# Optimization experiments

Measured on AMD Instinct MI355X. Metric: run time of the kernel, lower is better.

Reference implementation:

```python
import jax, jax.numpy as jnp
import numpy as np

IN_CH = 256
INTER_CH = 128
B, H, W = 8, 64, 64


def setup_inputs() -> dict:
    key = jax.random.key(0)
    ks = jax.random.split(key, 9)
    s_in = 1.0 / np.sqrt(IN_CH)
    s_int = 1.0 / np.sqrt(INTER_CH)
    return {
        "x": jax.random.normal(ks[0], (B, IN_CH, H, W), dtype=jnp.float32),
        "g_w": jax.random.normal(ks[1], (INTER_CH, IN_CH), dtype=jnp.float32) * s_in,
        "g_b": jax.random.normal(ks[2], (INTER_CH,), dtype=jnp.float32) * s_in,
        "theta_w": jax.random.normal(ks[3], (INTER_CH, IN_CH), dtype=jnp.float32) * s_in,
        "theta_b": jax.random.normal(ks[4], (INTER_CH,), dtype=jnp.float32) * s_in,
        "phi_w": jax.random.normal(ks[5], (INTER_CH, IN_CH), dtype=jnp.float32) * s_in,
        "phi_b": jax.random.normal(ks[6], (INTER_CH,), dtype=jnp.float32) * s_in,
        "W_w": jax.random.normal(ks[7], (IN_CH, INTER_CH), dtype=jnp.float32) * s_int,
        "W_b": jax.random.normal(ks[8], (IN_CH,), dtype=jnp.float32) * s_int,
    }


def _conv1x1(x, w, b):
    # x: [B,C,H,W], w: [O,C], b: [O] -> [B,O,H,W]
    return jnp.einsum("bchw,oc->bohw", x, w) + b[None, :, None, None]


def reference(x, g_w, g_b, theta_w, theta_b, phi_w, phi_b, W_w, W_b):
    b, c, h, w = x.shape
    n = h * w
    ic = g_w.shape[0]
    # 1x1 conv projections, flattened over spatial positions
    g_x = _conv1x1(x, g_w, g_b).reshape(b, ic, n).transpose(0, 2, 1)      # [B,N,ic]
    theta_x = _conv1x1(x, theta_w, theta_b).reshape(b, ic, n).transpose(0, 2, 1)  # [B,N,ic]
    phi_x = _conv1x1(x, phi_w, phi_b).reshape(b, ic, n)                   # [B,ic,N]
    f = jnp.einsum("bnc,bcm->bnm", theta_x, phi_x)                        # [B,N,N]
    # NOTE: original uses F.softmax(f, dim=1) -> normalize over axis 1 (rows)
    f_div_C = jax.nn.softmax(f, axis=1)
    y = jnp.einsum("bnm,bmc->bnc", f_div_C, g_x)                          # [B,N,ic]
    y = y.transpose(0, 2, 1).reshape(b, ic, h, w)                         # [B,ic,H,W]
    W_y = _conv1x1(y, W_w, W_b)                                           # [B,C,H,W]
    return W_y + x
```

## Files before the change

kernel.cpp:

```cpp
#include <hip/hip_runtime.h>
#include <hip/hip_bf16.h>


#define IC   128
#define CIN  256
#define NPOS 4096
#define NB   8

typedef _Float16 f16;
typedef __attribute__((ext_vector_type(8))) _Float16 f16x8;
typedef __attribute__((ext_vector_type(4))) _Float16 f16x4;
typedef __attribute__((ext_vector_type(4))) float f32x4;
typedef __attribute__((ext_vector_type(4))) float fvec4;
typedef __attribute__((ext_vector_type(2))) unsigned int u32x2;

#define MFMA16(a, b, c) __builtin_amdgcn_mfma_f32_16x16x32_f16((a), (b), (c), 0, 0, 0)
#define EXP2(x) __builtin_amdgcn_exp2f(x)

__global__ __launch_bounds__(256) void k_prep_w(
    const float* __restrict__ gw, const float* __restrict__ tw, const float* __restrict__ pw,
    const float* __restrict__ Ww, f16* __restrict__ wAll, f16* __restrict__ Wc)
{
    const int idx = (blockIdx.x * 256 + threadIdx.x) * 4;
    if (idx < 384 * 256) {
        const int row = idx >> 8, col = idx & 255;
        const float* src = (row < 128) ? (gw + row * 256)
                         : (row < 256) ? (tw + (row - 128) * 256)
                                       : (pw + (row - 256) * 256);
        fvec4 v = *reinterpret_cast<const fvec4*>(src + col);
        f16x4 o = { (f16)v[0], (f16)v[1], (f16)v[2], (f16)v[3] };
        *reinterpret_cast<f16x4*>(wAll + idx) = o;
    } else {
        const int j = idx - 384 * 256;
        fvec4 v = *reinterpret_cast<const fvec4*>(Ww + j);
        f16x4 o = { (f16)v[0], (f16)v[1], (f16)v[2], (f16)v[3] };
        *reinterpret_cast<f16x4*>(Wc + j) = o;
    }
}

__global__ __launch_bounds__(256) void k_split_x(
    const float* __restrict__ x, f16* __restrict__ xT)
{
    __shared__ float tile[64][65];
    const int b  = blockIdx.z;
    const int c0 = blockIdx.y * 64;
    const int n0 = blockIdx.x * 64;
    const int t  = threadIdx.x;
    {
        const int cc = t >> 4, nn = (t & 15) * 4;
        const float* src = x + ((size_t)b * CIN + c0) * NPOS + n0;
#pragma unroll
        for (int p = 0; p < 4; ++p) {
            fvec4 v = *reinterpret_cast<const fvec4*>(src + (size_t)(cc + p * 16) * NPOS + nn);
            tile[cc + p * 16][nn + 0] = v[0];
            tile[cc + p * 16][nn + 1] = v[1];
            tile[cc + p * 16][nn + 2] = v[2];
            tile[cc + p * 16][nn + 3] = v[3];
        }
    }
    __syncthreads();
    {
        const int c4 = (t & 15) * 4, nr = t >> 4;
#pragma unroll
        for (int p = 0; p < 4; ++p) {
            const int n = nr + p * 16;
            f16x4 o = { (f16)tile[c4 + 0][n], (f16)tile[c4 + 1][n],
                        (f16)tile[c4 + 2][n], (f16)tile[c4 + 3][n] };
            *reinterpret_cast<f16x4*>(xT + ((size_t)b * NPOS + n0 + n) * CIN + c0 + c4) = o;
        }
    }
}

__global__ __launch_bounds__(256) void k_proj(
    const f16* __restrict__ xT, const f16* __restrict__ wAll,
    const float* __restrict__ gb, const float* __restrict__ tb, const float* __restrict__ pb,
    f16* __restrict__ th, f16* __restrict__ ph, f16* __restrict__ gT)
{
    const int w    = threadIdx.x >> 6;
    const int lane = threadIdx.x & 63;
    const int lrow = lane & 15;
    const int kg   = lane >> 4;
    const int b    = blockIdx.z;
    const int c0   = blockIdx.y * 64;
    const int n0   = blockIdx.x * 256 + w * 64;

    const f16* X = xT + (size_t)b * NPOS * CIN;

    f32x4 acc[4][4] = {};
#pragma unroll
    for (int ks = 0; ks < 8; ++ks) {
        const int k = ks * 32 + kg * 8;
        f16x8 a[4], bv[4];
#pragma unroll
        for (int i = 0; i < 4; ++i) {
            a[i]  = *reinterpret_cast<const f16x8*>(wAll + (size_t)(c0 + i * 16 + lrow) * CIN + k);
            bv[i] = *reinterpret_cast<const f16x8*>(X + (size_t)(n0 + i * 16 + lrow) * CIN + k);
        }
#pragma unroll
        for (int i = 0; i < 4; ++i)
#pragma unroll
            for (int j = 0; j < 4; ++j)
                acc[i][j] = MFMA16(a[i], bv[j], acc[i][j]);
    }
    const int set = c0 >> 7;
    if (set == 0) {
#pragma unroll
        for (int i = 0; i < 4; ++i) {
            const int c = c0 + i * 16 + kg * 4;
#pragma unroll
            for (int j = 0; j < 4; ++j) {
                const int n = n0 + j * 16 + lrow;
#pragma unroll
                for (int r = 0; r < 4; ++r)
                    gT[((size_t)b * IC + c + r) * NPOS + n] = (f16)(acc[i][j][r] + gb[c + r]);
            }
        }
    } else {
        const float* Bi = (set == 1) ? tb : pb;
        f16* dst = (set == 1) ? th : ph;
        const int cl0 = (c0 & 127);
#pragma unroll
        for (int i = 0; i < 4; ++i) {
            const int c = cl0 + i * 16 + kg * 4;
#pragma unroll
            for (int j = 0; j < 4; ++j) {
                const int n = n0 + j * 16 + lrow;
                f16x4 o = { (f16)(acc[i][j][0] + Bi[c + 0]), (f16)(acc[i][j][1] + Bi[c + 1]),
                            (f16)(acc[i][j][2] + Bi[c + 2]), (f16)(acc[i][j][3] + Bi[c + 3]) };
                *reinterpret_cast<f16x4*>(dst + ((size_t)b * NPOS + n) * IC + c) = o;
            }
        }
    }
}

__global__ __launch_bounds__(256, 4) void k_gemm1(
    const f16* __restrict__ th, const f16* __restrict__ ph,
    f16* __restrict__ Ep, float* __restrict__ lmax, float* __restrict__ lsum, int b0)
{
    __shared__ f16 Alds[128 * 64];
    __shared__ f16 Blds[128 * 64];
    const int t    = threadIdx.x;
    const int w    = t >> 6;
    const int lane = t & 63;
    const int lrow = lane & 15;
    const int kg   = lane >> 4;
    const int wm   = w & 1;
    const int wn   = w >> 1;
    const int swz  = (blockIdx.x & 7) * 512 + (blockIdx.x >> 3);
    const int bi   = swz >> 10;
    const int rest = swz & 1023;
    const int mblk = rest & 31;
    const int nblk = rest >> 5;

    const f16* Ag = ph + (size_t)(b0 + bi) * NPOS * IC + (size_t)(mblk * 128) * IC;
    const f16* Bg = th + (size_t)(b0 + bi) * NPOS * IC + (size_t)(nblk * 128) * IC;

    const int trow = t >> 3;
    const int tc   = t & 7;

    f32x4 acc[4][4] = {};
#pragma unroll
    for (int h = 0; h < 2; ++h) {
        if (h) __syncthreads();
#pragma unroll
        for (int it = 0; it < 4; ++it) {
            const int row = trow + it * 32;
            const int cs  = tc ^ (row & 7);
            *reinterpret_cast<f16x8*>(&Alds[row * 64 + cs * 8]) =
                *reinterpret_cast<const f16x8*>(Ag + (size_t)row * IC + h * 64 + tc * 8);
            *reinterpret_cast<f16x8*>(&Blds[row * 64 + cs * 8]) =
                *reinterpret_cast<const f16x8*>(Bg + (size_t)row * IC + h * 64 + tc * 8);
        }
        __syncthreads();
#pragma unroll
        for (int ks = 0; ks < 2; ++ks) {
            f16x8 a[4], bv[4];
#pragma unroll
            for (int i = 0; i < 4; ++i) {
                const int mr = wm * 64 + i * 16 + lrow;
                const int cs = (ks * 4 + kg) ^ (mr & 7);
                a[i] = *reinterpret_cast<const f16x8*>(&Alds[mr * 64 + cs * 8]);
            }
#pragma unroll
            for (int j = 0; j < 4; ++j) {
                const int nr = wn * 64 + j * 16 + lrow;
                const int cs = (ks * 4 + kg) ^ (nr & 7);
                bv[j] = *reinterpret_cast<const f16x8*>(&Blds[nr * 64 + cs * 8]);
            }
#pragma unroll
            for (int i = 0; i < 4; ++i)
#pragma unroll
                for (int j = 0; j < 4; ++j)
                    acc[i][j] = MFMA16(a[i], bv[j], acc[i][j]);
        }
    }

    const int m0 = mblk * 128 + wm * 64;
    const int n0 = nblk * 128 + wn * 64;
    f16* eb = Ep + (size_t)bi * NPOS * NPOS;
    const float L2E = 1.4426950408889634f;

    f32x4 cm[4], ncml[4];
#pragma unroll
    for (int i = 0; i < 4; ++i)
#pragma unroll
        for (int r = 0; r < 4; ++r) {
            float c = fmaxf(fmaxf(acc[i][0][r], acc[i][1][r]),
                            fmaxf(acc[i][2][r], acc[i][3][r]));
            c = fmaxf(c, __shfl_xor(c, 1));
            c = fmaxf(c, __shfl_xor(c, 2));
            c = fmaxf(c, __shfl_xor(c, 4));
            c = fmaxf(c, __shfl_xor(c, 8));
            cm[i][r] = c;
            ncml[i][r] = -c * L2E;
        }

    f32x4 s[4] = {};
#pragma unroll
    for (int j = 0; j < 4; ++j) {
        f16* rowp = eb + (size_t)(n0 + j * 16 + lrow) * NPOS + m0 + kg * 4;
#pragma unroll
        for (int i = 0; i < 4; ++i) {
            float e0 = EXP2(__builtin_fmaf(acc[i][j][0], L2E, ncml[i][0]));
            float e1 = EXP2(__builtin_fmaf(acc[i][j][1], L2E, ncml[i][1]));
            float e2 = EXP2(__builtin_fmaf(acc[i][j][2], L2E, ncml[i][2]));
            float e3 = EXP2(__builtin_fmaf(acc[i][j][3], L2E, ncml[i][3]));
            s[i][0] += e0; s[i][1] += e1; s[i][2] += e2; s[i][3] += e3;
            u32x2 o = { __builtin_bit_cast(unsigned int, __builtin_amdgcn_cvt_pkrtz(e0, e1)),
                        __builtin_bit_cast(unsigned int, __builtin_amdgcn_cvt_pkrtz(e2, e3)) };
            *reinterpret_cast<u32x2*>(rowp + i * 16) = o;
        }
    }

    const int rowblk = nblk * 2 + wn;
#pragma unroll
    for (int i = 0; i < 4; ++i)
#pragma unroll
        for (int r = 0; r < 4; ++r) {
            float ss = s[i][r];
            ss += __shfl_xor(ss, 1);
            ss += __shfl_xor(ss, 2);
            ss += __shfl_xor(ss, 4);
            ss += __shfl_xor(ss, 8);
            if (lrow == 0) {
                const size_t off = ((size_t)bi * 64 + rowblk) * NPOS + m0 + i * 16 + kg * 4 + r;
                lmax[off] = cm[i][r];
                lsum[off] = ss;
            }
        }
}

__global__ __launch_bounds__(256) void k_prep(
    const float* __restrict__ lmax, const float* __restrict__ lsum,
    const f16* __restrict__ gT, f16* __restrict__ sca, f16* __restrict__ gs, int b0)
{
    const float L2E = 1.4426950408889634f;
    const int bi = blockIdx.y;
    const int m  = blockIdx.x * 256 + threadIdx.x;
    const float* lm = lmax + (size_t)bi * 64 * NPOS;
    const float* ls = lsum + (size_t)bi * 64 * NPOS;
    float cm = -3.0e38f;
#pragma unroll 8
    for (int rb = 0; rb < 64; ++rb)
        cm = fmaxf(cm, lm[(size_t)rb * NPOS + m]);
    float s = 0.f;
    f16* scab = sca + (size_t)bi * 64 * NPOS;
#pragma unroll 8
    for (int rb = 0; rb < 64; ++rb) {
        float e = EXP2((lm[(size_t)rb * NPOS + m] - cm) * L2E);
        s += e * ls[(size_t)rb * NPOS + m];
        scab[(size_t)rb * NPOS + m] = (f16)e;
    }
    const float rc = 1.0f / s;
    const f16* gb = gT + (size_t)(b0 + bi) * IC * NPOS;
    f16* gsb = gs + (size_t)bi * IC * NPOS;
#pragma unroll 8
    for (int c = 0; c < IC; ++c)
        gsb[(size_t)c * NPOS + m] = (f16)((float)gb[(size_t)c * NPOS + m] * rc);
}

__global__ __launch_bounds__(256, 2) void k_gemm2(
    const f16* __restrict__ Ep, const f16* __restrict__ sca,
    const f16* __restrict__ gs, f16* __restrict__ partial)
{
    __shared__ f16 Elds[2][128 * 64];
    __shared__ f16 Glds[2][128 * 64];
    const int t    = threadIdx.x;
    const int w    = t >> 6;
    const int lane = t & 63;
    const int lrow = lane & 15;
    const int kg   = lane >> 4;
    const int wc   = w & 1;
    const int wn   = w >> 1;
    const int swz  = (blockIdx.x & 7) * 64 + (blockIdx.x >> 3);
    const int bi   = swz >> 7;
    const int rest = swz & 127;
    const int kc   = rest & 3;
    const int nblk = rest >> 2;

    const f16* Eg  = Ep + (size_t)bi * NPOS * NPOS + (size_t)(nblk * 128) * NPOS + kc * 1024;
    const f16* Gg  = gs + (size_t)bi * IC * NPOS + kc * 1024;
    const int  rb  = nblk * 2 + wn;
    const f16* srow = sca + ((size_t)bi * 64 + rb) * NPOS + kc * 1024;

    const int trow = t >> 3;
    const int tc   = t & 7;

    f16x8 pe[4], pg[4];
#pragma unroll
    for (int it = 0; it < 4; ++it) {
        const int row = trow + it * 32;
        pe[it] = *reinterpret_cast<const f16x8*>(Eg + (size_t)row * NPOS + tc * 8);
        pg[it] = *reinterpret_cast<const f16x8*>(Gg + (size_t)row * NPOS + tc * 8);
    }

    f32x4 acc[4][4] = {};
    for (int sc = 0; sc < 16; ++sc) {
        const int cur = sc & 1;
#pragma unroll
        for (int it = 0; it < 4; ++it) {
            const int row = trow + it * 32;
            const int cs  = tc ^ (row & 7);
            *reinterpret_cast<f16x8*>(&Elds[cur][row * 64 + cs * 8]) = pe[it];
            *reinterpret_cast<f16x8*>(&Glds[cur][row * 64 + cs * 8]) = pg[it];
        }
        if (sc < 15) {
#pragma unroll
            for (int it = 0; it < 4; ++it) {
                const int row = trow + it * 32;
                pe[it] = *reinterpret_cast<const f16x8*>(Eg + (size_t)row * NPOS + (sc + 1) * 64 + tc * 8);
                pg[it] = *reinterpret_cast<const f16x8*>(Gg + (size_t)row * NPOS + (sc + 1) * 64 + tc * 8);
            }
        }
        __syncthreads();

#pragma unroll
        for (int ks = 0; ks < 2; ++ks) {
            f16x8 sv = *reinterpret_cast<const f16x8*>(srow + sc * 64 + ks * 32 + kg * 8);
            f16x8 a[4], ev[4];
#pragma unroll
            for (int i = 0; i < 4; ++i) {
                const int cr = wc * 64 + i * 16 + lrow;
                const int cs = (ks * 4 + kg) ^ (cr & 7);
                a[i] = *reinterpret_cast<const f16x8*>(&Glds[cur][cr * 64 + cs * 8]);
            }
#pragma unroll
            for (int j = 0; j < 4; ++j) {
                const int nr = wn * 64 + j * 16 + lrow;
                const int cs = (ks * 4 + kg) ^ (nr & 7);
                ev[j] = *reinterpret_cast<const f16x8*>(&Elds[cur][nr * 64 + cs * 8]) * sv;
            }
#pragma unroll
            for (int i = 0; i < 4; ++i)
#pragma unroll
                for (int j = 0; j < 4; ++j)
                    acc[i][j] = MFMA16(a[i], ev[j], acc[i][j]);
        }
    }

    f16* pb = partial + ((size_t)bi * 4 + kc) * NPOS * IC;
    const int n0 = nblk * 128 + wn * 64;
    const int c0 = wc * 64;
#pragma unroll
    for (int j = 0; j < 4; ++j) {
        f16* rowp = pb + (size_t)(n0 + j * 16 + lrow) * IC + c0 + kg * 4;
#pragma unroll
        for (int i = 0; i < 4; ++i) {
            f16x4 o = { (f16)acc[i][j][0], (f16)acc[i][j][1],
                        (f16)acc[i][j][2], (f16)acc[i][j][3] };
            *reinterpret_cast<f16x4*>(rowp + i * 16) = o;
        }
    }
}

__global__ __launch_bounds__(256) void k_reduce(
    const f16* __restrict__ partial, f16* __restrict__ yT, int b0)
{
    const int bi  = blockIdx.y;
    const int idx = blockIdx.x * 256 + threadIdx.x;
    const f16x8* p = reinterpret_cast<const f16x8*>(partial + (size_t)bi * 4 * NPOS * IC);
    float s[8] = {};
#pragma unroll
    for (int kc = 0; kc < 4; ++kc) {
        f16x8 v = p[(size_t)kc * (NPOS * IC / 8) + idx];
#pragma unroll
        for (int k = 0; k < 8; ++k)
            s[k] += (float)v[k];
    }
    f16x8 o;
#pragma unroll
    for (int k = 0; k < 8; ++k)
        o[k] = (f16)s[k];
    *reinterpret_cast<f16x8*>(yT + (size_t)(b0 + bi) * NPOS * IC + (size_t)idx * 8) = o;
}

__global__ __launch_bounds__(256) void k_conv(
    const float* __restrict__ x, const f16* __restrict__ Wc, const float* __restrict__ Wb,
    const f16* __restrict__ yT, float* __restrict__ out)
{
    const int w    = threadIdx.x >> 6;
    const int lane = threadIdx.x & 63;
    const int lrow = lane & 15;
    const int kg   = lane >> 4;
    const int gwid = blockIdx.x * 4 + w;
    const int ob   = gwid & 3;
    const int nb   = (gwid >> 2) & 63;
    const int b    = gwid >> 8;
    const int o0   = ob * 64;
    const int n0   = nb * 64;

    const f16* Y = yT + (size_t)b * NPOS * IC;
    f32x4 acc[4][4] = {};
#pragma unroll
    for (int ks = 0; ks < 4; ++ks) {
        const int k = ks * 32 + kg * 8;
        f16x8 a[4], bv[4];
#pragma unroll
        for (int i = 0; i < 4; ++i) {
            a[i]  = *reinterpret_cast<const f16x8*>(Wc + (size_t)(o0 + i * 16 + lrow) * IC + k);
            bv[i] = *reinterpret_cast<const f16x8*>(Y + (size_t)(n0 + i * 16 + lrow) * IC + k);
        }
#pragma unroll
        for (int i = 0; i < 4; ++i)
#pragma unroll
            for (int j = 0; j < 4; ++j)
                acc[i][j] = MFMA16(a[i], bv[j], acc[i][j]);
    }
#pragma unroll
    for (int i = 0; i < 4; ++i) {
        const int o = o0 + i * 16 + kg * 4;
#pragma unroll
        for (int j = 0; j < 4; ++j) {
            const int n = n0 + j * 16 + lrow;
#pragma unroll
            for (int r = 0; r < 4; ++r) {
                const size_t off = ((size_t)b * CIN + o + r) * NPOS + n;
                out[off] = acc[i][j][r] + x[off] + Wb[o + r];
            }
        }
    }
}

extern "C" void kernel_launch(void* const* d_in, const int* in_sizes, int n_in,
                              void* d_out, int out_size, void* d_ws, size_t ws_size,
                              hipStream_t stream)
{
    const float* x  = (const float*)d_in[0];
    const float* gw = (const float*)d_in[1];
    const float* gb = (const float*)d_in[2];
    const float* tw = (const float*)d_in[3];
    const float* tb = (const float*)d_in[4];
    const float* pw = (const float*)d_in[5];
    const float* pb = (const float*)d_in[6];
    const float* Ww = (const float*)d_in[7];
    const float* Wb = (const float*)d_in[8];
    float* out = (float*)d_out;

    char* ws = (char*)d_ws;
    size_t off = 0;
    auto alloc = [&](size_t bytes) -> char* {
        char* p = ws + off;
        off += (bytes + 255) & ~(size_t)255;
        return p;
    };
    f16* xT   = (f16*)alloc((size_t)NB * NPOS * CIN * 2);
    f16* wAll = (f16*)alloc((size_t)384 * 256 * 2);
    f16* Wc   = (f16*)alloc((size_t)CIN * IC * 2);
    f16* th   = (f16*)alloc((size_t)NB * NPOS * IC * 2);
    f16* ph   = (f16*)alloc((size_t)NB * NPOS * IC * 2);
    f16* gT   = (f16*)alloc((size_t)NB * NPOS * IC * 2);
    f16* Ep   = (f16*)alloc((size_t)4 * NPOS * NPOS * 2);
    float* lmax = (float*)alloc((size_t)4 * 64 * NPOS * 4);
    float* lsum = (float*)alloc((size_t)4 * 64 * NPOS * 4);
    f16* sca  = (f16*)alloc((size_t)4 * 64 * NPOS * 2);
    f16* gs   = (f16*)alloc((size_t)4 * IC * NPOS * 2);
    f16* partial = (f16*)alloc((size_t)4 * 4 * NPOS * IC * 2);
    f16* yT   = (f16*)alloc((size_t)NB * NPOS * IC * 2);

    k_prep_w<<<128, 256, 0, stream>>>(gw, tw, pw, Ww, wAll, Wc);
    k_split_x<<<dim3(64, 4, 8), 256, 0, stream>>>(x, xT);
    k_proj<<<dim3(16, 6, 8), 256, 0, stream>>>(xT, wAll, gb, tb, pb, th, ph, gT);

    for (int b0 = 0; b0 < NB; b0 += 4) {
        k_gemm1<<<4096, 256, 0, stream>>>(th, ph, Ep, lmax, lsum, b0);
        k_prep<<<dim3(16, 4), 256, 0, stream>>>(lmax, lsum, gT, sca, gs, b0);
        k_gemm2<<<512, 256, 0, stream>>>(Ep, sca, gs, partial);
        k_reduce<<<dim3(256, 4), 256, 0, stream>>>(partial, yT, b0);
    }
    k_conv<<<dim3(512), 256, 0, stream>>>(x, Wc, Wb, yT, out);
}
```

Baseline: 332.9 us.

## Fuse x transpose into projection and split-K reduce into output conv

Removes the separate x transpose/convert kernel. The projection kernel now loads fp32 x directly, converts it to fp16 and stores it in a swizzled LDS tile shared by six waves that cover all 384 output channels. It also drops the split-K reduce kernel: gemm2 writes per-batch partials for all 8 batches, and the final conv sums the four partial slices while loading its operand. This cuts two launches and the xT/yT round trips through global memory. In exchange the partial buffer is larger, the conv reads four times more Y data, and the partials are summed in fp16 rather than fp32.

```diff
diff --git a/kernel.cpp b/kernel.cpp
--- a/kernel.cpp
+++ b/kernel.cpp
@@ -38,53 +38,38 @@
     }
 }
 
-__global__ __launch_bounds__(256) void k_split_x(
-    const float* __restrict__ x, f16* __restrict__ xT)
-{
-    __shared__ float tile[64][65];
-    const int b  = blockIdx.z;
-    const int c0 = blockIdx.y * 64;
-    const int n0 = blockIdx.x * 64;
-    const int t  = threadIdx.x;
-    {
-        const int cc = t >> 4, nn = (t & 15) * 4;
-        const float* src = x + ((size_t)b * CIN + c0) * NPOS + n0;
-#pragma unroll
-        for (int p = 0; p < 4; ++p) {
-            fvec4 v = *reinterpret_cast<const fvec4*>(src + (size_t)(cc + p * 16) * NPOS + nn);
-            tile[cc + p * 16][nn + 0] = v[0];
-            tile[cc + p * 16][nn + 1] = v[1];
-            tile[cc + p * 16][nn + 2] = v[2];
-            tile[cc + p * 16][nn + 3] = v[3];
-        }
-    }
-    __syncthreads();
-    {
-        const int c4 = (t & 15) * 4, nr = t >> 4;
-#pragma unroll
-        for (int p = 0; p < 4; ++p) {
-            const int n = nr + p * 16;
-            f16x4 o = { (f16)tile[c4 + 0][n], (f16)tile[c4 + 1][n],
-                        (f16)tile[c4 + 2][n], (f16)tile[c4 + 3][n] };
-            *reinterpret_cast<f16x4*>(xT + ((size_t)b * NPOS + n0 + n) * CIN + c0 + c4) = o;
-        }
-    }
-}
-
-__global__ __launch_bounds__(256) void k_proj(
-    const f16* __restrict__ xT, const f16* __restrict__ wAll,
+__global__ __launch_bounds__(384) void k_proj(
+    const float* __restrict__ x, const f16* __restrict__ wAll,
     const float* __restrict__ gb, const float* __restrict__ tb, const float* __restrict__ pb,
     f16* __restrict__ th, f16* __restrict__ ph, f16* __restrict__ gT)
 {
-    const int w    = threadIdx.x >> 6;
-    const int lane = threadIdx.x & 63;
+    __shared__ f16 Xl[64 * 256];
+    const int t  = threadIdx.x;
+    const int b  = blockIdx.y;
+    const int n0 = blockIdx.x * 64;
+
+    if (t < 256) {
+        const int nq = (t & 15) * 4;
+        const float* xb = x + (size_t)b * CIN * NPOS + n0 + nq;
+#pragma unroll
+        for (int it = 0; it < 16; ++it) {
+            const int c = (t >> 4) + it * 16;
+            fvec4 v = *reinterpret_cast<const fvec4*>(xb + (size_t)c * NPOS);
+#pragma unroll
+            for (int d = 0; d < 4; ++d) {
+                const int row = nq + d;
+                const int cs  = (c >> 3) ^ (row & 7);
+                Xl[row * 256 + cs * 8 + (c & 7)] = (f16)v[d];
+            }
+        }
+    }
+    __syncthreads();
+
+    const int w    = t >> 6;
+    const int lane = t & 63;
     const int lrow = lane & 15;
     const int kg   = lane >> 4;
-    const int b    = blockIdx.z;
-    const int c0   = blockIdx.y * 64;
-    const int n0   = blockIdx.x * 256 + w * 64;
-
-    const f16* X = xT + (size_t)b * NPOS * CIN;
+    const int c0   = w * 64;
 
     f32x4 acc[4][4] = {};
 #pragma unroll
@@ -92,9 +77,13 @@
         const int k = ks * 32 + kg * 8;
         f16x8 a[4], bv[4];
 #pragma unroll
-        for (int i = 0; i < 4; ++i) {
-            a[i]  = *reinterpret_cast<const f16x8*>(wAll + (size_t)(c0 + i * 16 + lrow) * CIN + k);
-            bv[i] = *reinterpret_cast<const f16x8*>(X + (size_t)(n0 + i * 16 + lrow) * CIN + k);
+        for (int i = 0; i < 4; ++i)
+            a[i] = *reinterpret_cast<const f16x8*>(wAll + (size_t)(c0 + i * 16 + lrow) * CIN + k);
+#pragma unroll
+        for (int j = 0; j < 4; ++j) {
+            const int row = j * 16 + lrow;
+            const int cs  = (k >> 3) ^ (row & 7);
+            bv[j] = *reinterpret_cast<const f16x8*>(&Xl[row * 256 + cs * 8]);
         }
 #pragma unroll
         for (int i = 0; i < 4; ++i)
@@ -281,7 +270,7 @@
 
 __global__ __launch_bounds__(256, 2) void k_gemm2(
     const f16* __restrict__ Ep, const f16* __restrict__ sca,
-    const f16* __restrict__ gs, f16* __restrict__ partial)
+    const f16* __restrict__ gs, f16* __restrict__ partial, int b0)
 {
     __shared__ f16 Elds[2][128 * 64];
     __shared__ f16 Glds[2][128 * 64];
@@ -358,7 +347,7 @@
         }
     }
 
-    f16* pb = partial + ((size_t)bi * 4 + kc) * NPOS * IC;
+    f16* pb = partial + ((size_t)(b0 + bi) * 4 + kc) * NPOS * IC;
     const int n0 = nblk * 128 + wn * 64;
     const int c0 = wc * 64;
 #pragma unroll
@@ -373,30 +362,9 @@
     }
 }
 
-__global__ __launch_bounds__(256) void k_reduce(
-    const f16* __restrict__ partial, f16* __restrict__ yT, int b0)
-{
-    const int bi  = blockIdx.y;
-    const int idx = blockIdx.x * 256 + threadIdx.x;
-    const f16x8* p = reinterpret_cast<const f16x8*>(partial + (size_t)bi * 4 * NPOS * IC);
-    float s[8] = {};
-#pragma unroll
-    for (int kc = 0; kc < 4; ++kc) {
-        f16x8 v = p[(size_t)kc * (NPOS * IC / 8) + idx];
-#pragma unroll
-        for (int k = 0; k < 8; ++k)
-            s[k] += (float)v[k];
-    }
-    f16x8 o;
-#pragma unroll
-    for (int k = 0; k < 8; ++k)
-        o[k] = (f16)s[k];
-    *reinterpret_cast<f16x8*>(yT + (size_t)(b0 + bi) * NPOS * IC + (size_t)idx * 8) = o;
-}
-
 __global__ __launch_bounds__(256) void k_conv(
     const float* __restrict__ x, const f16* __restrict__ Wc, const float* __restrict__ Wb,
-    const f16* __restrict__ yT, float* __restrict__ out)
+    const f16* __restrict__ partial, float* __restrict__ out)
 {
     const int w    = threadIdx.x >> 6;
     const int lane = threadIdx.x & 63;
@@ -409,7 +377,8 @@
     const int o0   = ob * 64;
     const int n0   = nb * 64;
 
-    const f16* Y = yT + (size_t)b * NPOS * IC;
+    const f16* Y = partial + (size_t)b * 4 * NPOS * IC;
+    const size_t SL = (size_t)NPOS * IC;
     f32x4 acc[4][4] = {};
 #pragma unroll
     for (int ks = 0; ks < 4; ++ks) {
@@ -418,7 +387,12 @@
 #pragma unroll
         for (int i = 0; i < 4; ++i) {
             a[i]  = *reinterpret_cast<const f16x8*>(Wc + (size_t)(o0 + i * 16 + lrow) * IC + k);
-            bv[i] = *reinterpret_cast<const f16x8*>(Y + (size_t)(n0 + i * 16 + lrow) * IC + k);
+            const f16* yr = Y + (size_t)(n0 + i * 16 + lrow) * IC + k;
+            f16x8 v0 = *reinterpret_cast<const f16x8*>(yr);
+            f16x8 v1 = *reinterpret_cast<const f16x8*>(yr + SL);
+            f16x8 v2 = *reinterpret_cast<const f16x8*>(yr + 2 * SL);
+            f16x8 v3 = *reinterpret_cast<const f16x8*>(yr + 3 * SL);
+            bv[i] = (v0 + v1) + (v2 + v3);
         }
 #pragma unroll
         for (int i = 0; i < 4; ++i)
@@ -463,7 +437,6 @@
         off += (bytes + 255) & ~(size_t)255;
         return p;
     };
-    f16* xT   = (f16*)alloc((size_t)NB * NPOS * CIN * 2);
     f16* wAll = (f16*)alloc((size_t)384 * 256 * 2);
     f16* Wc   = (f16*)alloc((size_t)CIN * IC * 2);
     f16* th   = (f16*)alloc((size_t)NB * NPOS * IC * 2);
@@ -474,18 +447,15 @@
     float* lsum = (float*)alloc((size_t)4 * 64 * NPOS * 4);
     f16* sca  = (f16*)alloc((size_t)4 * 64 * NPOS * 2);
     f16* gs   = (f16*)alloc((size_t)4 * IC * NPOS * 2);
-    f16* partial = (f16*)alloc((size_t)4 * 4 * NPOS * IC * 2);
-    f16* yT   = (f16*)alloc((size_t)NB * NPOS * IC * 2);
+    f16* partial = (f16*)alloc((size_t)NB * 4 * NPOS * IC * 2);
 
     k_prep_w<<<128, 256, 0, stream>>>(gw, tw, pw, Ww, wAll, Wc);
-    k_split_x<<<dim3(64, 4, 8), 256, 0, stream>>>(x, xT);
-    k_proj<<<dim3(16, 6, 8), 256, 0, stream>>>(xT, wAll, gb, tb, pb, th, ph, gT);
+    k_proj<<<dim3(64, 8), 384, 0, stream>>>(x, wAll, gb, tb, pb, th, ph, gT);
 
     for (int b0 = 0; b0 < NB; b0 += 4) {
         k_gemm1<<<4096, 256, 0, stream>>>(th, ph, Ep, lmax, lsum, b0);
         k_prep<<<dim3(16, 4), 256, 0, stream>>>(lmax, lsum, gT, sca, gs, b0);
-        k_gemm2<<<512, 256, 0, stream>>>(Ep, sca, gs, partial);
-        k_reduce<<<dim3(256, 4), 256, 0, stream>>>(partial, yT, b0);
-    }
-    k_conv<<<dim3(512), 256, 0, stream>>>(x, Wc, Wb, yT, out);
-}
+        k_gemm2<<<512, 256, 0, stream>>>(Ep, sca, gs, partial, b0);
+    }
+    k_conv<<<dim3(512), 256, 0, stream>>>(x, Wc, Wb, partial, out);
+}
```

After: 307.8 us, median of 2. -7.5%, faster.
